# Optimization experiments

Measured on AMD Instinct MI355X. Metric: run time of the kernel, lower is better.

The kernel has to match this reference:

```python
import jax, jax.numpy as jnp
import numpy as np

B, S, D = 32, 1024, 1024
A = 256           # adapter_size
E = 16            # num_domains
LN_EPS = 1e-5


def setup_inputs() -> dict:
    key = jax.random.key(0)
    ks = jax.random.split(key, 10)
    s = lambda fan_in: 1.0 / np.sqrt(fan_in)
    return {
        'hidden_states': jax.random.normal(ks[0], (B, S, D), dtype=jnp.float32),
        'domain_id': jax.random.randint(ks[1], (B,), 0, E, dtype=jnp.int64),
        'down_W': jax.random.uniform(ks[2], (A, D), jnp.float32, -s(D), s(D)),
        'down_b': jax.random.uniform(ks[3], (A,), jnp.float32, -s(D), s(D)),
        'up_W': jax.random.uniform(ks[4], (D, A), jnp.float32, -s(A), s(A)),
        'up_b': jax.random.uniform(ks[5], (D,), jnp.float32, -s(A), s(A)),
        'expert_W': jax.random.uniform(ks[6], (E, A, A), jnp.float32, -s(A), s(A)),
        'expert_b': jax.random.uniform(ks[7], (E, A), jnp.float32, -s(A), s(A)),
        'domain_emb': jax.random.normal(ks[8], (E, A), dtype=jnp.float32),
        'ln_gamma': jnp.ones((D,), jnp.float32),
        'ln_beta': jnp.zeros((D,), jnp.float32),
    }


def reference(hidden_states, domain_id, down_W, down_b, up_W, up_b,
              expert_W, expert_b, domain_emb, ln_gamma, ln_beta):
    residual = hidden_states
    # down projection + exact GELU (torch nn.GELU default)
    hidden = jnp.einsum('bsd,ad->bsa', hidden_states, down_W) + down_b
    hidden = jax.nn.gelu(hidden, approximate=False)
    # per-sample expert linear: gather each sample's expert weight, batched GEMM
    valid = (domain_id >= 0) & (domain_id < E)
    idx = jnp.clip(domain_id, 0, E - 1)
    Wsel = expert_W[idx]                      # [B, A, A]
    bsel = expert_b[idx]                      # [B, A]
    expert_out = jnp.einsum('bsa,boa->bso', hidden, Wsel) + bsel[:, None, :]
    domain_output = jnp.where(valid[:, None, None], expert_out, hidden)
    # add domain embedding broadcast over seq
    hidden = domain_output + domain_emb[idx][:, None, :]
    # up projection (dropout is identity at inference)
    hidden = jnp.einsum('bsa,da->bsd', hidden, up_W) + up_b
    # layer norm over last dim
    x = hidden + residual
    mu = jnp.mean(x, axis=-1, keepdims=True)
    var = jnp.mean(jnp.square(x - mu), axis=-1, keepdims=True)
    return (x - mu) * jax.lax.rsqrt(var + LN_EPS) * ln_gamma + ln_beta
```

## Files before the change

### kernel.cpp

```cpp
#include <hip/hip_runtime.h>
#include <hip/hip_bf16.h>
#include <math.h>

#define D_DIM 1024
#define A_DIM 256
#define E_NUM 16

typedef __attribute__((ext_vector_type(8))) short short8;
typedef __attribute__((ext_vector_type(4))) float f32x4;

__device__ __forceinline__ short f2bs(float x) {
    __hip_bfloat16 h = __float2bfloat16(x);
    return __builtin_bit_cast(short, h);
}
__device__ __forceinline__ float bs2f(short s) {
    __hip_bfloat16 h = __builtin_bit_cast(__hip_bfloat16, s);
    return __bfloat162float(h);
}
__device__ __forceinline__ float gelu_exact(float x) {
    return 0.5f * x * (1.0f + erff(x * 0.70710678118654752f));
}
__device__ __forceinline__ void gload_lds16(const void* g, void* l) {
    __builtin_amdgcn_global_load_lds(
        (const __attribute__((address_space(1))) void*)g,
        (__attribute__((address_space(3))) void*)l, 16, 0, 0);
}
__device__ __forceinline__ short8 pack8(float4 u, float4 v) {
    short8 pk;
    pk[0] = f2bs(u.x); pk[1] = f2bs(u.y); pk[2] = f2bs(u.z); pk[3] = f2bs(u.w);
    pk[4] = f2bs(v.x); pk[5] = f2bs(v.y); pk[6] = f2bs(v.z); pk[7] = f2bs(v.w);
    return pk;
}

__global__ __launch_bounds__(256) void k_cast_w(
    const float* __restrict__ Wd, const float* __restrict__ Wu,
    const float* __restrict__ eW,
    short* __restrict__ WdB, short* __restrict__ WuB, short* __restrict__ eWB)
{
    unsigned i = blockIdx.x * 256 + threadIdx.x;
    if (i < 131072) {
        const float4* s = (const float4*)eW;
        ((short8*)eWB)[i] = pack8(s[2 * (size_t)i], s[2 * (size_t)i + 1]);
    } else if (i < 163840) {
        unsigned j = i - 131072;
        const float4* s = (const float4*)Wd;
        ((short8*)WdB)[j] = pack8(s[2 * (size_t)j], s[2 * (size_t)j + 1]);
    } else {
        unsigned j = i - 163840;
        const float4* s = (const float4*)Wu;
        ((short8*)WuB)[j] = pack8(s[2 * (size_t)j], s[2 * (size_t)j + 1]);
    }
}

__global__ __launch_bounds__(256, 2) void k_down_expert(
    const float* __restrict__ X, const short* __restrict__ WdB,
    const float* __restrict__ bd, const short* __restrict__ eWB,
    const float* __restrict__ eb, const float* __restrict__ emb,
    const int* __restrict__ domain_id, short* __restrict__ H2)
{
    __shared__ short As[64][72];
    __shared__ short Bs[256][64];
    __shared__ short Hs[64][264];
    const int tid  = threadIdx.x;
    const int lane = tid & 63;
    const int w    = tid >> 6;
    const int quad = lane >> 4, cid = lane & 15;
    const int m0 = blockIdx.x * 64;

    const int samp = m0 >> 10;
    const int id = domain_id[samp];
    const bool valid = (id >= 0) && (id < E_NUM);
    const int idc = id < 0 ? 0 : (id > E_NUM - 1 ? E_NUM - 1 : id);

    f32x4 acc[4][4];
    #pragma unroll
    for (int i = 0; i < 4; i++)
        #pragma unroll
        for (int j = 0; j < 4; j++) acc[i][j] = (f32x4)(0.f);

    for (int kt = 0; kt < D_DIM; kt += 64) {
        #pragma unroll
        for (int p = 0; p < 8; p++) {
            int jj = tid + p * 256;
            int r = jj >> 3, c = (jj & 7) * 8;
            gload_lds16(WdB + (size_t)r * D_DIM + kt + c, &Bs[r][c]);
        }
        #pragma unroll
        for (int p = 0; p < 2; p++) {
            int jj = tid + p * 256;
            int r = jj >> 3, c = (jj & 7) * 8;
            const float4* src = (const float4*)(X + (size_t)(m0 + r) * D_DIM + kt + c);
            *(short8*)&As[r][c] = pack8(src[0], src[1]);
        }
        __syncthreads();
        #pragma unroll
        for (int kk = 0; kk < 2; kk++) {
            short8 a[4], b[4];
            #pragma unroll
            for (int i = 0; i < 4; i++)
                a[i] = *(const short8*)&As[i * 16 + cid][kk * 32 + quad * 8];
            #pragma unroll
            for (int j = 0; j < 4; j++)
                b[j] = *(const short8*)&Bs[w * 64 + j * 16 + cid][kk * 32 + quad * 8];
            #pragma unroll
            for (int i = 0; i < 4; i++)
                #pragma unroll
                for (int j = 0; j < 4; j++)
                    acc[i][j] = __builtin_amdgcn_mfma_f32_16x16x32_bf16(
                        a[i], b[j], acc[i][j], 0, 0, 0);
        }
        __syncthreads();
    }

    #pragma unroll
    for (int j = 0; j < 4; j++) {
        int col = w * 64 + j * 16 + cid;
        float bdv = bd[col];
        #pragma unroll
        for (int i = 0; i < 4; i++)
            #pragma unroll
            for (int r = 0; r < 4; r++)
                Hs[i * 16 + quad * 4 + r][col] = f2bs(gelu_exact(acc[i][j][r] + bdv));
    }

    f32x4 acc2[4][4];
    #pragma unroll
    for (int i = 0; i < 4; i++)
        #pragma unroll
        for (int j = 0; j < 4; j++) acc2[i][j] = (f32x4)(0.f);

    const short* Bsrc = eWB + (size_t)idc * A_DIM * A_DIM;
    for (int kt = 0; kt < A_DIM; kt += 64) {
        #pragma unroll
        for (int p = 0; p < 8; p++) {
            int jj = tid + p * 256;
            int r = jj >> 3, c = (jj & 7) * 8;
            gload_lds16(Bsrc + (size_t)r * A_DIM + kt + c, &Bs[r][c]);
        }
        __syncthreads();
        #pragma unroll
        for (int kk = 0; kk < 2; kk++) {
            short8 a[4], b[4];
            #pragma unroll
            for (int i = 0; i < 4; i++)
                a[i] = *(const short8*)&Hs[i * 16 + cid][kt + kk * 32 + quad * 8];
            #pragma unroll
            for (int j = 0; j < 4; j++)
                b[j] = *(const short8*)&Bs[w * 64 + j * 16 + cid][kk * 32 + quad * 8];
            #pragma unroll
            for (int i = 0; i < 4; i++)
                #pragma unroll
                for (int j = 0; j < 4; j++)
                    acc2[i][j] = __builtin_amdgcn_mfma_f32_16x16x32_bf16(
                        a[i], b[j], acc2[i][j], 0, 0, 0);
        }
        __syncthreads();
    }

    #pragma unroll
    for (int j = 0; j < 4; j++) {
        int col = w * 64 + j * 16 + cid;
        float ebv = eb[idc * A_DIM + col];
        float ev  = emb[idc * A_DIM + col];
        #pragma unroll
        for (int i = 0; i < 4; i++)
            #pragma unroll
            for (int r = 0; r < 4; r++) {
                int rl = i * 16 + quad * 4 + r;
                float base;
                if (valid) base = acc2[i][j][r] + ebv;
                else       base = bs2f(Hs[rl][col]);
                H2[(size_t)(m0 + rl) * A_DIM + col] = f2bs(base + ev);
            }
    }
}

__global__ __launch_bounds__(1024, 4) void k_up_ln(
    const short* __restrict__ H2, const short* __restrict__ WuB,
    const float* __restrict__ ub, const float* __restrict__ X,
    const float* __restrict__ gamma, const float* __restrict__ beta,
    float* __restrict__ out)
{
    __shared__ short As[32][64];
    __shared__ float redS[16][32], red2[16][32];
    __shared__ float muS[32], rsS[32];
    const int tid  = threadIdx.x;
    const int lane = tid & 63;
    const int w    = tid >> 6;
    const int quad = lane >> 4, cid = lane & 15;
    const int m0 = blockIdx.x * 32;
    const int nb = w * 64;

    f32x4 acc[2][4];
    #pragma unroll
    for (int mf = 0; mf < 2; mf++)
        #pragma unroll
        for (int j = 0; j < 4; j++) acc[mf][j] = (f32x4)(0.f);

    const short* bbase = WuB + (size_t)(nb + cid) * A_DIM + quad * 8;

    for (int kt = 0; kt < A_DIM; kt += 64) {
        if (tid < 256) {
            int r = tid >> 3, c = (tid & 7) * 8;
            gload_lds16(H2 + (size_t)(m0 + r) * A_DIM + kt + c, &As[r][c]);
        }
        __syncthreads();
        #pragma unroll
        for (int kk = 0; kk < 2; kk++) {
            short8 a0 = *(const short8*)&As[cid][kk * 32 + quad * 8];
            short8 a1 = *(const short8*)&As[16 + cid][kk * 32 + quad * 8];
            #pragma unroll
            for (int j = 0; j < 4; j++) {
                short8 b = *(const short8*)(bbase + (size_t)(j * 16) * A_DIM + kt + kk * 32);
                acc[0][j] = __builtin_amdgcn_mfma_f32_16x16x32_bf16(a0, b, acc[0][j], 0, 0, 0);
                acc[1][j] = __builtin_amdgcn_mfma_f32_16x16x32_bf16(a1, b, acc[1][j], 0, 0, 0);
            }
        }
        __syncthreads();
    }

    float s1[2][4], s2[2][4];
    #pragma unroll
    for (int mf = 0; mf < 2; mf++)
        #pragma unroll
        for (int r = 0; r < 4; r++) { s1[mf][r] = 0.f; s2[mf][r] = 0.f; }
    #pragma unroll
    for (int j = 0; j < 4; j++) {
        int col = nb + j * 16 + cid;
        float ubv = ub[col];
        #pragma unroll
        for (int mf = 0; mf < 2; mf++)
            #pragma unroll
            for (int r = 0; r < 4; r++) {
                int row = m0 + mf * 16 + quad * 4 + r;
                float x = acc[mf][j][r] + ubv + X[(size_t)row * D_DIM + col];
                acc[mf][j][r] = x;
                s1[mf][r] += x;
                s2[mf][r] += x * x;
            }
    }
    #pragma unroll
    for (int mf = 0; mf < 2; mf++)
        #pragma unroll
        for (int r = 0; r < 4; r++) {
            float a = s1[mf][r], b = s2[mf][r];
            #pragma unroll
            for (int off = 1; off < 16; off <<= 1) {
                a += __shfl_xor(a, off, 64);
                b += __shfl_xor(b, off, 64);
            }
            if (cid == 0) {
                int rl = mf * 16 + quad * 4 + r;
                redS[w][rl] = a;
                red2[w][rl] = b;
            }
        }
    __syncthreads();
    if (tid < 32) {
        float S = 0.f, Q = 0.f;
        #pragma unroll
        for (int ww = 0; ww < 16; ww++) { S += redS[ww][tid]; Q += red2[ww][tid]; }
        float mu = S * (1.0f / 1024.0f);
        float var = Q * (1.0f / 1024.0f) - mu * mu;
        muS[tid] = mu;
        rsS[tid] = rsqrtf(var + 1e-5f);
    }
    __syncthreads();
    #pragma unroll
    for (int j = 0; j < 4; j++) {
        int col = nb + j * 16 + cid;
        float g = gamma[col], be = beta[col];
        #pragma unroll
        for (int mf = 0; mf < 2; mf++)
            #pragma unroll
            for (int r = 0; r < 4; r++) {
                int rl = mf * 16 + quad * 4 + r;
                out[(size_t)(m0 + rl) * D_DIM + col] =
                    (acc[mf][j][r] - muS[rl]) * rsS[rl] * g + be;
            }
    }
}

extern "C" void kernel_launch(void* const* d_in, const int* in_sizes, int n_in,
                              void* d_out, int out_size, void* d_ws, size_t ws_size,
                              hipStream_t stream) {
    const float* hs  = (const float*)d_in[0];
    const int*   did = (const int*)d_in[1];
    const float* dW  = (const float*)d_in[2];
    const float* db  = (const float*)d_in[3];
    const float* uW  = (const float*)d_in[4];
    const float* ub  = (const float*)d_in[5];
    const float* eW  = (const float*)d_in[6];
    const float* ebv = (const float*)d_in[7];
    const float* emb = (const float*)d_in[8];
    const float* gam = (const float*)d_in[9];
    const float* bet = (const float*)d_in[10];
    float* out = (float*)d_out;

    char* ws = (char*)d_ws;
    short* WdB = (short*)(ws);
    short* WuB = (short*)(ws + (1u << 19));
    short* eWB = (short*)(ws + (1u << 20));
    short* H2  = (short*)(ws + (3u << 20));

    k_cast_w     <<<768, 256, 0, stream>>>(dW, uW, eW, WdB, WuB, eWB);
    k_down_expert<<<512, 256, 0, stream>>>(hs, WdB, db, eWB, ebv, emb, did, H2);
    k_up_ln      <<<1024, 1024, 0, stream>>>(H2, WuB, ub, hs, gam, bet, out);
}
```

Baseline: 371.5 us.

## Swizzle expert/down weight LDS tiles and preload H2 and residual in up-LN kernel

```diff
diff --git a/kernel.cpp b/kernel.cpp
--- a/kernel.cpp
+++ b/kernel.cpp
@@ -82,8 +82,10 @@
         #pragma unroll
         for (int p = 0; p < 8; p++) {
             int jj = tid + p * 256;
-            int r = jj >> 3, c = (jj & 7) * 8;
-            gload_lds16(WdB + (size_t)r * D_DIM + kt + c, &Bs[r][c]);
+            int r = jj >> 3;
+            int cg = (((jj & 7) ^ (r & 7)) * 8);
+            int cl = (jj & 7) * 8;
+            gload_lds16(WdB + (size_t)r * D_DIM + kt + cg, &Bs[r][cl]);
         }
         #pragma unroll
         for (int p = 0; p < 2; p++) {
@@ -101,7 +103,8 @@
                 a[i] = *(const short8*)&As[i * 16 + cid][kk * 32 + quad * 8];
             #pragma unroll
             for (int j = 0; j < 4; j++)
-                b[j] = *(const short8*)&Bs[w * 64 + j * 16 + cid][kk * 32 + quad * 8];
+                b[j] = *(const short8*)&Bs[w * 64 + j * 16 + cid]
+                                         [(kk * 32 + quad * 8) ^ ((cid & 7) * 8)];
             #pragma unroll
             for (int i = 0; i < 4; i++)
                 #pragma unroll
@@ -134,8 +137,10 @@
         #pragma unroll
         for (int p = 0; p < 8; p++) {
             int jj = tid + p * 256;
-            int r = jj >> 3, c = (jj & 7) * 8;
-            gload_lds16(Bsrc + (size_t)r * A_DIM + kt + c, &Bs[r][c]);
+            int r = jj >> 3;
+            int cg = (((jj & 7) ^ (r & 7)) * 8);
+            int cl = (jj & 7) * 8;
+            gload_lds16(Bsrc + (size_t)r * A_DIM + kt + cg, &Bs[r][cl]);
         }
         __syncthreads();
         #pragma unroll
@@ -146,7 +151,8 @@
                 a[i] = *(const short8*)&Hs[i * 16 + cid][kt + kk * 32 + quad * 8];
             #pragma unroll
             for (int j = 0; j < 4; j++)
-                b[j] = *(const short8*)&Bs[w * 64 + j * 16 + cid][kk * 32 + quad * 8];
+                b[j] = *(const short8*)&Bs[w * 64 + j * 16 + cid]
+                                         [(kk * 32 + quad * 8) ^ ((cid & 7) * 8)];
             #pragma unroll
             for (int i = 0; i < 4; i++)
                 #pragma unroll
@@ -181,7 +187,7 @@
     const float* __restrict__ gamma, const float* __restrict__ beta,
     float* __restrict__ out)
 {
-    __shared__ short As[32][64];
+    __shared__ short As[32][264];
     __shared__ float redS[16][32], red2[16][32];
     __shared__ float muS[32], rsS[32];
     const int tid  = threadIdx.x;
@@ -191,6 +197,24 @@
     const int m0 = blockIdx.x * 32;
     const int nb = w * 64;
 
+    const int pr = tid >> 5, pc = (tid & 31) * 8;
+    short8 pv = *(const short8*)(H2 + (size_t)(m0 + pr) * A_DIM + pc);
+
+    float xres[4][2][4];
+    #pragma unroll
+    for (int j = 0; j < 4; j++) {
+        int col = nb + j * 16 + cid;
+        #pragma unroll
+        for (int mf = 0; mf < 2; mf++)
+            #pragma unroll
+            for (int r = 0; r < 4; r++)
+                xres[j][mf][r] =
+                    X[(size_t)(m0 + mf * 16 + quad * 4 + r) * D_DIM + col];
+    }
+
+    *(short8*)&As[pr][pc] = pv;
+    __syncthreads();
+
     f32x4 acc[2][4];
     #pragma unroll
     for (int mf = 0; mf < 2; mf++)
@@ -199,24 +223,20 @@
 
     const short* bbase = WuB + (size_t)(nb + cid) * A_DIM + quad * 8;
 
-    for (int kt = 0; kt < A_DIM; kt += 64) {
-        if (tid < 256) {
-            int r = tid >> 3, c = (tid & 7) * 8;
-            gload_lds16(H2 + (size_t)(m0 + r) * A_DIM + kt + c, &As[r][c]);
-        }
-        __syncthreads();
+    #pragma unroll
+    for (int kt = 0; kt < 4; kt++) {
         #pragma unroll
         for (int kk = 0; kk < 2; kk++) {
-            short8 a0 = *(const short8*)&As[cid][kk * 32 + quad * 8];
-            short8 a1 = *(const short8*)&As[16 + cid][kk * 32 + quad * 8];
+            short8 a0 = *(const short8*)&As[cid][kt * 64 + kk * 32 + quad * 8];
+            short8 a1 = *(const short8*)&As[16 + cid][kt * 64 + kk * 32 + quad * 8];
             #pragma unroll
             for (int j = 0; j < 4; j++) {
-                short8 b = *(const short8*)(bbase + (size_t)(j * 16) * A_DIM + kt + kk * 32);
+                short8 b = *(const short8*)(bbase + (size_t)(j * 16) * A_DIM
+                                            + kt * 64 + kk * 32);
                 acc[0][j] = __builtin_amdgcn_mfma_f32_16x16x32_bf16(a0, b, acc[0][j], 0, 0, 0);
                 acc[1][j] = __builtin_amdgcn_mfma_f32_16x16x32_bf16(a1, b, acc[1][j], 0, 0, 0);
             }
         }
-        __syncthreads();
     }
 
     float s1[2][4], s2[2][4];
@@ -232,8 +252,7 @@
         for (int mf = 0; mf < 2; mf++)
             #pragma unroll
             for (int r = 0; r < 4; r++) {
-                int row = m0 + mf * 16 + quad * 4 + r;
-                float x = acc[mf][j][r] + ubv + X[(size_t)row * D_DIM + col];
+                float x = acc[mf][j][r] + ubv + xres[j][mf][r];
                 acc[mf][j][r] = x;
                 s1[mf][r] += x;
                 s2[mf][r] += x * x;
```

After: 389.1 us. 4.7% more time.
